# Kernel tuning notes

Hardware: AMD Instinct MI355X
Metric: run time of the kernel (lower is better)

Reference implementation:

```python
import jax, jax.numpy as jnp
import numpy as np

B, C, H, W = 8, 256, 64, 64
NH, KD, AG, PS, MIP = 8, 32, 64, 8, 8   # heads, key_dim, agent_num, pool_size, mip
EPS = 1e-5
SCALE = KD ** -0.5


def _bn(x, p):
    # p: [4, C] rows = (gamma, beta, mean, var); inference-mode BatchNorm2d, x: [B,C,H,W]
    g, b, m, v = p[0], p[1], p[2], p[3]
    inv = g * jax.lax.rsqrt(v + EPS)
    return x * inv[:, None, None] + (b - m * inv)[:, None, None]


def _conv1x1_bn(x, w, p):
    # 1x1 conv (no bias) + BN; act is Identity (the torch Conv act assignment is
    # overwritten by the else-branch, so even act='silu' ends up Identity)
    return _bn(jnp.einsum('bchw,oc->bohw', x, w), p)


def setup_inputs() -> dict:
    key = jax.random.key(0)
    ks = jax.random.split(key, 12)
    s = 0.05
    return {
        'x':       jax.random.normal(ks[0], (B, C, H, W), jnp.float32),
        'w_qkv':   jax.random.normal(ks[1], (3 * C, C), jnp.float32) * s,
        'bn_qkv':  jax.random.uniform(ks[2], (4, 3 * C), jnp.float32, 0.5, 1.5),
        'w_cv1':   jax.random.normal(ks[3], (MIP, C), jnp.float32) * s,
        'bn_cv1':  jax.random.uniform(ks[4], (4, MIP), jnp.float32, 0.5, 1.5),
        'w_cv2':   jax.random.normal(ks[5], (C, MIP), jnp.float32) * s,
        'bn_cv2':  jax.random.uniform(ks[6], (4, C), jnp.float32, 0.5, 1.5),
        'w_proj':  jax.random.normal(ks[7], (C, C), jnp.float32) * s,
        'bn_proj': jax.random.uniform(ks[8], (4, C), jnp.float32, 0.5, 1.5),
        'w_pe':    jax.random.normal(ks[9], (C, 1, 3, 3), jnp.float32) * s,
        'bn_pe':   jax.random.uniform(ks[10], (4, C), jnp.float32, 0.5, 1.5),
    }


def reference(x, w_qkv, bn_qkv, w_cv1, bn_cv1, w_cv2, bn_cv2,
              w_proj, bn_proj, w_pe, bn_pe):
    N = H * W
    qkv = _conv1x1_bn(x, w_qkv, bn_qkv)                     # [B,3C,H,W]
    q, k, v = jnp.split(qkv, 3, axis=1)                     # each [B,C,H,W]

    # direct == 'h': pool over W -> [B,C,H,1], SE-style gate via cv1->cv2, multiply
    a_k = k.mean(axis=3, keepdims=True)
    a_v = v.mean(axis=3, keepdims=True)
    k = _conv1x1_bn(_conv1x1_bn(a_k, w_cv1, bn_cv1), w_cv2, bn_cv2) * k
    v = _conv1x1_bn(_conv1x1_bn(a_v, w_cv1, bn_cv1), w_cv2, bn_cv2) * v

    # agent tokens: AdaptiveAvgPool2d to (PS,PS) == block-mean since H,W % PS == 0
    ap = q.reshape(B, C, PS, H // PS, PS, W // PS).mean(axis=(3, 5))  # [B,C,PS,PS]
    a = ap.reshape(B, NH, KD, AG)                            # [B,h,d,agent]

    qr = q.reshape(B, NH, KD, N)
    kr = k.reshape(B, NH, KD, N)
    vr = v.reshape(B, NH, KD, N)

    attn_k = jax.nn.softmax(jnp.einsum('bhda,bhdn->bhan', a, kr) * SCALE, axis=-1)  # [B,h,agent,N]
    attn = jnp.einsum('bhan,bhdn->bhad', attn_k, vr)                                # [B,h,agent,d]
    q_attn = jax.nn.softmax(jnp.einsum('bhdn,bhda->bhna', qr, a) * SCALE, axis=-1)  # [B,h,N,agent]
    out = jnp.einsum('bhna,bhad->bhdn', q_attn, attn).reshape(B, C, H, W)

    # depthwise 3x3 positional encoding on v, then BN
    pe = jax.lax.conv_general_dilated(
        v, w_pe, window_strides=(1, 1), padding='SAME',
        dimension_numbers=('NCHW', 'OIHW', 'NCHW'), feature_group_count=C)
    out = out + _bn(pe, bn_pe)

    return _conv1x1_bn(out, w_proj, bn_proj)
```

## Files before the change

### kernel.cpp

```cpp
#include <hip/hip_runtime.h>
#include <hip/hip_bf16.h>

#define NB 8
#define NC 256
#define NHW 4096
#define HDIM 64
#define WDIM 64
#define NHEAD 8
#define NKD 32
#define NAG 64
#define NMIP 8
#define NSPLIT 16
#define EPSF 1e-5f
#define FSCALE 0.17677669529663687f
#define SZQ ((size_t)NB * NC * NHW)

typedef __attribute__((ext_vector_type(8))) short bf16x8;
typedef __attribute__((ext_vector_type(8))) unsigned short u16x8;
typedef __attribute__((ext_vector_type(4))) unsigned short u16x4;
typedef __attribute__((ext_vector_type(4))) float f32x4;

__device__ __forceinline__ unsigned short f2bf(float f) {
    union { float f; unsigned u; } v; v.f = f;
    unsigned r = v.u + 0x7FFF + ((v.u >> 16) & 1);
    return (unsigned short)(r >> 16);
}
__device__ __forceinline__ float b2f(unsigned short u) {
    union { unsigned u32; float f; } v; v.u32 = ((unsigned)u) << 16; return v.f;
}
__device__ __forceinline__ void gload_lds16(const unsigned short* g, unsigned short* l) {
    __builtin_amdgcn_global_load_lds(
        (const __attribute__((address_space(1))) unsigned int*)g,
        (__attribute__((address_space(3))) unsigned int*)l, 16, 0, 0);
}

__global__ __launch_bounds__(256) void k_xpose(const float* __restrict__ x,
                                               unsigned short* __restrict__ xbt) {
    const int b = blockIdx.y;
    const int n0 = blockIdx.x * 64;
    const int tid = threadIdx.x;
    __shared__ unsigned short lt[64 * 258];

    #pragma unroll
    for (int it = 0; it < 4; ++it) {
        int c = it * 64 + (tid >> 2);
        int nq = (tid & 3) * 16;
        const float* xp = x + ((size_t)b * NC + c) * NHW + n0 + nq;
        float4 v0 = reinterpret_cast<const float4*>(xp)[0];
        float4 v1 = reinterpret_cast<const float4*>(xp)[1];
        float4 v2 = reinterpret_cast<const float4*>(xp)[2];
        float4 v3 = reinterpret_cast<const float4*>(xp)[3];
        float t[16] = {v0.x,v0.y,v0.z,v0.w, v1.x,v1.y,v1.z,v1.w,
                       v2.x,v2.y,v2.z,v2.w, v3.x,v3.y,v3.z,v3.w};
        #pragma unroll
        for (int i = 0; i < 16; ++i)
            lt[(nq + i) * 258 + c] = f2bf(t[i]);
    }
    __syncthreads();

    const int n = tid >> 2, cq = tid & 3;
    unsigned short* dst = xbt + ((size_t)b * NHW + n0 + n) * NC + cq * 64;
    #pragma unroll
    for (int v = 0; v < 8; ++v) {
        union { unsigned short u[8]; u16x8 w; } pk;
        #pragma unroll
        for (int i = 0; i < 8; ++i)
            pk.u[i] = lt[n * 258 + cq * 64 + v * 8 + i];
        *reinterpret_cast<u16x8*>(dst + v * 8) = pk.w;
    }
}

__global__ __launch_bounds__(256) void k_wcast(const float* __restrict__ wq,
                                               const float* __restrict__ wp,
                                               unsigned short* __restrict__ wqb,
                                               unsigned short* __restrict__ wpb) {
    const int i = (blockIdx.x * 256 + threadIdx.x) * 4;
    const int NQ = 768 * 256;
    if (i < NQ) {
        float4 v = *reinterpret_cast<const float4*>(wq + i);
        u16x4 u = {f2bf(v.x), f2bf(v.y), f2bf(v.z), f2bf(v.w)};
        *reinterpret_cast<u16x4*>(wqb + i) = u;
    } else {
        int j = i - NQ;
        float4 v = *reinterpret_cast<const float4*>(wp + j);
        u16x4 u = {f2bf(v.x), f2bf(v.y), f2bf(v.z), f2bf(v.w)};
        *reinterpret_cast<u16x4*>(wpb + j) = u;
    }
}

__global__ __launch_bounds__(256) void k_qkv(const unsigned short* __restrict__ xbt,
                                             const unsigned short* __restrict__ wb,
                                             const float* __restrict__ bnp,
                                             unsigned short* __restrict__ Qb,
                                             unsigned short* __restrict__ Kb,
                                             unsigned short* __restrict__ Vb,
                                             float* __restrict__ AMK,
                                             float* __restrict__ AMV) {
    const int b   = blockIdx.z;
    const int ocB = blockIdx.y * 128;
    const int nB  = blockIdx.x * 128;
    const int tid = threadIdx.x;
    const int wv  = tid >> 6, lane = tid & 63;
    const int wm = wv >> 1, wn = wv & 1;
    const int lm = lane & 15, lg = lane >> 4;

    __shared__ __align__(16) unsigned short S[2][8192];

    f32x4 acc[4][4];
    #pragma unroll
    for (int i = 0; i < 4; ++i)
        #pragma unroll
        for (int j = 0; j < 4; ++j)
            acc[i][j] = (f32x4){0.f, 0.f, 0.f, 0.f};

    const int srow = lane >> 2;
    const int kl = ((lane & 3) ^ ((lane >> 3) & 3)) * 8;
    const size_t agbase = (size_t)(ocB + wv * 32 + srow) * 256 + kl;
    const size_t bgbase = ((size_t)b * NHW + nB + wv * 32 + srow) * NC + kl;
    const int sw = (lm >> 1) & 3;

    auto STAGE = [&](int buf, int k0) {
        #pragma unroll
        for (int j = 0; j < 2; ++j) {
            gload_lds16(wb + agbase + (size_t)j * 16 * 256 + k0, &S[buf][wv * 1024 + j * 512]);
            gload_lds16(xbt + bgbase + (size_t)j * 16 * NC + k0, &S[buf][4096 + wv * 1024 + j * 512]);
        }
    };

    STAGE(0, 0);
    asm volatile("s_waitcnt vmcnt(0)" ::: "memory");
    __builtin_amdgcn_s_barrier();
    __builtin_amdgcn_sched_barrier(0);

    int cur = 0;
    for (int t = 0; t < 8; ++t) {
        if (t < 7) STAGE(cur ^ 1, (t + 1) * 32);

        const unsigned short* As = &S[cur][0];
        const unsigned short* Bs = &S[cur][4096];
        bf16x8 af[4], bfr[4];
        #pragma unroll
        for (int mi = 0; mi < 4; ++mi)
            af[mi] = *reinterpret_cast<const bf16x8*>(&As[(wm * 64 + mi * 16 + lm) * 32 + (lg ^ sw) * 8]);
        #pragma unroll
        for (int ni = 0; ni < 4; ++ni)
            bfr[ni] = *reinterpret_cast<const bf16x8*>(&Bs[(wn * 64 + ni * 16 + lm) * 32 + (lg ^ sw) * 8]);
        #pragma unroll
        for (int mi = 0; mi < 4; ++mi)
            #pragma unroll
            for (int ni = 0; ni < 4; ++ni)
                acc[mi][ni] = __builtin_amdgcn_mfma_f32_16x16x32_bf16(af[mi], bfr[ni], acc[mi][ni], 0, 0, 0);

        if (t < 7) {
            asm volatile("s_waitcnt vmcnt(0)" ::: "memory");
            __builtin_amdgcn_s_barrier();
            __builtin_amdgcn_sched_barrier(0);
            cur ^= 1;
        }
    }

    const int h_sp = (nB >> 6) + wn;
    unsigned short* wep = &S[0][0] + wv * 1152;
    #pragma unroll
    for (int mi = 0; mi < 4; ++mi) {
        const int ocrow = ocB + wm * 64 + mi * 16;
        #pragma unroll
        for (int r = 0; r < 4; ++r) {
            int lo = lg * 4 + r;
            int oc = ocrow + lo;
            float g = bnp[0 * 768 + oc], be = bnp[1 * 768 + oc];
            float m = bnp[2 * 768 + oc], vv = bnp[3 * 768 + oc];
            float inv = g * rsqrtf(vv + EPSF);
            float bias = be - m * inv;
            #pragma unroll
            for (int ni = 0; ni < 4; ++ni)
                wep[lo * 72 + ni * 16 + lm] = f2bf(acc[mi][ni][r] * inv + bias);
        }
        #pragma unroll
        for (int it = 0; it < 2; ++it) {
            int row = it * 8 + (lane >> 3);
            int seg = lane & 7;
            u16x8 v = *reinterpret_cast<const u16x8*>(&wep[row * 72 + seg * 8]);
            int oc = ocrow + row;
            unsigned short* base; int oc2;
            if (oc < 256)      { base = Qb; oc2 = oc; }
            else if (oc < 512) { base = Kb; oc2 = oc - 256; }
            else               { base = Vb; oc2 = oc - 512; }
            *reinterpret_cast<u16x8*>(base + ((size_t)b * NC + oc2) * NHW + nB + wn * 64 + seg * 8) = v;
            if (ocrow >= 256) {
                float s = 0.f;
                #pragma unroll
                for (int j = 0; j < 8; ++j) s += b2f(v[j]);
                s += __shfl_xor(s, 1);
                s += __shfl_xor(s, 2);
                s += __shfl_xor(s, 4);
                if (seg == 0) {
                    float* am = (oc < 512) ? AMK : AMV;
                    am[((size_t)b * HDIM + h_sp) * NC + oc2] = s * (1.0f / 64.0f);
                }
            }
        }
    }
}

__global__ __launch_bounds__(256) void k_gatecomp(const float* __restrict__ AMK,
                                                  const float* __restrict__ AMV,
                                                  const float* __restrict__ w1,
                                                  const float* __restrict__ bn1,
                                                  const float* __restrict__ w2,
                                                  const float* __restrict__ bn2,
                                                  float* __restrict__ GK,
                                                  float* __restrict__ GV) {
    const int b = blockIdx.x >> 6;
    const int h = blockIdx.x & 63;
    const int c = threadIdx.x;
    __shared__ float am[NC];
    __shared__ float m1[NMIP];
    for (int pass = 0; pass < 2; ++pass) {
        am[c] = (pass ? AMV : AMK)[((size_t)b * HDIM + h) * NC + c];
        __syncthreads();
        if (c < NMIP) {
            float t = 0.f;
            for (int cc = 0; cc < NC; ++cc) t += w1[c * NC + cc] * am[cc];
            float g = bn1[0 * NMIP + c], be = bn1[1 * NMIP + c];
            float mm = bn1[2 * NMIP + c], vv = bn1[3 * NMIP + c];
            float inv = g * rsqrtf(vv + EPSF);
            m1[c] = t * inv + (be - mm * inv);
        }
        __syncthreads();
        {
            float t = 0.f;
            #pragma unroll
            for (int j = 0; j < NMIP; ++j) t += w2[c * NMIP + j] * m1[j];
            float g = bn2[0 * NC + c], be = bn2[1 * NC + c];
            float mm = bn2[2 * NC + c], vv = bn2[3 * NC + c];
            float inv = g * rsqrtf(vv + EPSF);
            (pass ? GV : GK)[((size_t)b * NC + c) * HDIM + h] = t * inv + (be - mm * inv);
        }
        __syncthreads();
    }
}

__global__ __launch_bounds__(64) void k_pool(const unsigned short* __restrict__ Q,
                                             float* __restrict__ A_) {
    const int bc = blockIdx.x;
    const int ag = threadIdx.x;
    const int ph = ag >> 3, pw = ag & 7;
    const unsigned short* src = Q + (size_t)bc * NHW;
    float s = 0.f;
    #pragma unroll
    for (int i = 0; i < 8; ++i) {
        u16x8 v = *reinterpret_cast<const u16x8*>(&src[(ph * 8 + i) * WDIM + pw * 8]);
        #pragma unroll
        for (int j = 0; j < 8; ++j) s += b2f(v[j]);
    }
    A_[(size_t)bc * NAG + ag] = s * (1.0f / 64.0f);
}

__global__ __launch_bounds__(256) void k_attn_part(const unsigned short* __restrict__ K,
                                                   const unsigned short* __restrict__ V,
                                                   const float* __restrict__ A_,
                                                   const float* __restrict__ GK,
                                                   const float* __restrict__ GV,
                                                   float* __restrict__ Pm,
                                                   float* __restrict__ Pl,
                                                   float* __restrict__ Pacc) {
    const int bh = blockIdx.x >> 4;
    const int ns = blockIdx.x & (NSPLIT - 1);
    const int b = bh >> 3, h = bh & 7;
    const int tid = threadIdx.x;
    const int wv = tid >> 6, lane = tid & 63;
    const int lm = lane & 15, lg = lane >> 4;

    __shared__ unsigned short a_s[64 * 40];
    __shared__ unsigned short kt_s[64 * 40];
    __shared__ unsigned short vt_s[32 * 72];
    __shared__ unsigned short Ps[64 * 72];

    {
        int d = tid >> 3, ag0 = (tid & 7) * 8;
        const float* ap = A_ + ((size_t)(b * NC + h * NKD + d)) * NAG + ag0;
        float4 v0 = reinterpret_cast<const float4*>(ap)[0];
        float4 v1 = reinterpret_cast<const float4*>(ap)[1];
        float t8[8] = {v0.x, v0.y, v0.z, v0.w, v1.x, v1.y, v1.z, v1.w};
        #pragma unroll
        for (int i = 0; i < 8; ++i)
            a_s[(ag0 + i) * 40 + d] = f2bf(t8[i] * FSCALE);
    }

    float mrow[4], lrow[4];
    f32x4 acc[2];
    #pragma unroll
    for (int r = 0; r < 4; ++r) { mrow[r] = -1e30f; lrow[r] = 0.f; }
    acc[0] = (f32x4){0.f, 0.f, 0.f, 0.f};
    acc[1] = (f32x4){0.f, 0.f, 0.f, 0.f};

    const int colbase = ns * (NHW / NSPLIT);
    const unsigned short* Kp = K + (size_t)(b * NC + h * NKD) * NHW + colbase;
    const unsigned short* Vp = V + (size_t)(b * NC + h * NKD) * NHW + colbase;
    const int sd = tid >> 3;
    const size_t gbase = ((size_t)(b * NC + h * NKD + sd)) * HDIM;
    __syncthreads();

    for (int nt = 0; nt < 4; ++nt) {
        const int gh = ns * 4 + nt;
        {
            int c0 = tid & 7;
            float gk = GK[gbase + gh];
            const unsigned short* kp = Kp + (size_t)sd * NHW + nt * 64 + c0;
            #pragma unroll
            for (int i = 0; i < 8; ++i)
                kt_s[(c0 + 8 * i) * 40 + sd] = f2bf(b2f(kp[8 * i]) * gk);
        }
        {
            int c0 = (tid & 7) * 8;
            float gv = GV[gbase + gh];
            const unsigned short* vp = Vp + (size_t)sd * NHW + nt * 64 + c0;
            u16x8 vr = *reinterpret_cast<const u16x8*>(vp);
            union { unsigned short u[8]; u16x8 v; } pk;
            #pragma unroll
            for (int i = 0; i < 8; ++i) pk.u[i] = f2bf(b2f(vr[i]) * gv);
            *reinterpret_cast<u16x8*>(&vt_s[sd * 72 + c0]) = pk.v;
        }
        __syncthreads();

        f32x4 s[4];
        {
            bf16x8 af = *reinterpret_cast<const bf16x8*>(&a_s[(wv * 16 + lm) * 40 + lg * 8]);
            #pragma unroll
            for (int ni = 0; ni < 4; ++ni) {
                bf16x8 kf = *reinterpret_cast<const bf16x8*>(&kt_s[(ni * 16 + lm) * 40 + lg * 8]);
                s[ni] = __builtin_amdgcn_mfma_f32_16x16x32_bf16(
                    af, kf, (f32x4){0.f, 0.f, 0.f, 0.f}, 0, 0, 0);
            }
        }

        float fsc[4];
        #pragma unroll
        for (int r = 0; r < 4; ++r) {
            float mx = fmaxf(fmaxf(s[0][r], s[1][r]), fmaxf(s[2][r], s[3][r]));
            mx = fmaxf(mx, __shfl_xor(mx, 1));
            mx = fmaxf(mx, __shfl_xor(mx, 2));
            mx = fmaxf(mx, __shfl_xor(mx, 4));
            mx = fmaxf(mx, __shfl_xor(mx, 8));
            float mnew = fmaxf(mrow[r], mx);
            fsc[r] = __expf(mrow[r] - mnew);
            mrow[r] = mnew;
            int agrow = wv * 16 + lg * 4 + r;
            float ps = 0.f;
            #pragma unroll
            for (int ni = 0; ni < 4; ++ni) {
                float p = __expf(s[ni][r] - mnew);
                Ps[agrow * 72 + ni * 16 + lm] = f2bf(p);
                ps += p;
            }
            ps += __shfl_xor(ps, 1);
            ps += __shfl_xor(ps, 2);
            ps += __shfl_xor(ps, 4);
            ps += __shfl_xor(ps, 8);
            lrow[r] = lrow[r] * fsc[r] + ps;
        }
        #pragma unroll
        for (int ni = 0; ni < 2; ++ni)
            #pragma unroll
            for (int r = 0; r < 4; ++r)
                acc[ni][r] *= fsc[r];
        __syncthreads();

        #pragma unroll
        for (int kk = 0; kk < 2; ++kk) {
            bf16x8 pa = *reinterpret_cast<const bf16x8*>(&Ps[(wv * 16 + lm) * 72 + kk * 32 + lg * 8]);
            #pragma unroll
            for (int ni = 0; ni < 2; ++ni) {
                bf16x8 vb = *reinterpret_cast<const bf16x8*>(&vt_s[(ni * 16 + lm) * 72 + kk * 32 + lg * 8]);
                acc[ni] = __builtin_amdgcn_mfma_f32_16x16x32_bf16(pa, vb, acc[ni], 0, 0, 0);
            }
        }
        __syncthreads();
    }

    const size_t pbase = (size_t)(bh * NSPLIT + ns) * NAG;
    #pragma unroll
    for (int r = 0; r < 4; ++r) {
        int ag = wv * 16 + lg * 4 + r;
        #pragma unroll
        for (int ni = 0; ni < 2; ++ni)
            Pacc[(pbase + ag) * NKD + ni * 16 + lm] = acc[ni][r];
        if (lm == 0) {
            Pm[pbase + ag] = mrow[r];
            Pl[pbase + ag] = lrow[r];
        }
    }
}

__global__ __launch_bounds__(256) void k_attn_comb(const float* __restrict__ Pm,
                                                   const float* __restrict__ Pl,
                                                   const float* __restrict__ Pacc,
                                                   float* __restrict__ AT) {
    const int bh = blockIdx.x;
    const int tid = threadIdx.x;
    const int ag = tid >> 2, jg = tid & 3;
    float m = -1e30f;
    #pragma unroll
    for (int ns = 0; ns < NSPLIT; ++ns)
        m = fmaxf(m, Pm[(size_t)(bh * NSPLIT + ns) * NAG + ag]);
    float l = 0.f;
    float acc[8] = {};
    for (int ns = 0; ns < NSPLIT; ++ns) {
        size_t pb = (size_t)(bh * NSPLIT + ns) * NAG + ag;
        float f = __expf(Pm[pb] - m);
        l += Pl[pb] * f;
        const float* pp = Pacc + pb * NKD + jg * 8;
        #pragma unroll
        for (int i = 0; i < 8; ++i) acc[i] += pp[i] * f;
    }
    float linv = 1.0f / l;
    #pragma unroll
    for (int i = 0; i < 8; ++i)
        AT[((size_t)bh * NAG + ag) * NKD + jg * 8 + i] = acc[i] * linv;
}

__global__ __launch_bounds__(256) void k_qattn(const unsigned short* __restrict__ Q,
                                               const float* __restrict__ A_,
                                               const float* __restrict__ AT,
                                               unsigned short* __restrict__ O1t) {
    const int bh = blockIdx.y;
    const int b = bh >> 3, h = bh & 7;
    const int n0 = blockIdx.x * 128;
    const int tid = threadIdx.x;
    const int wv = tid >> 6, lane = tid & 63;
    const int lm = lane & 15, lg = lane >> 4;

    __shared__ unsigned short Qs[128][40];
    __shared__ unsigned short Ags[64][40];
    __shared__ unsigned short ATs[32][72];
    __shared__ unsigned short Ps[128][72];

    const unsigned short* Qbase = Q + ((size_t)b * NC + h * NKD) * NHW;

    {
        int d = tid >> 3, nb_ = (tid & 7) * 16;
        const unsigned short* qp = Qbase + (size_t)d * NHW + n0 + nb_;
        u16x8 v0 = *reinterpret_cast<const u16x8*>(qp);
        u16x8 v1 = *reinterpret_cast<const u16x8*>(qp + 8);
        #pragma unroll
        for (int i = 0; i < 8; ++i) Qs[nb_ + i][d] = v0[i];
        #pragma unroll
        for (int i = 0; i < 8; ++i) Qs[nb_ + 8 + i][d] = v1[i];
    }
    if (tid < 128) {
        int d = tid >> 2, ag0 = (tid & 3) * 16;
        const float* ap = A_ + ((size_t)(b * NC + h * NKD + d)) * NAG + ag0;
        #pragma unroll
        for (int i = 0; i < 16; ++i) Ags[ag0 + i][d] = f2bf(ap[i] * FSCALE);
    }
    if (tid < 128) {
        int ag = tid >> 1, d0 = (tid & 1) * 16;
        const float* atp = AT + ((size_t)bh * NAG + ag) * NKD + d0;
        #pragma unroll
        for (int i = 0; i < 16; ++i) ATs[d0 + i][ag] = f2bf(atp[i]);
    }
    __syncthreads();

    f32x4 s[2][4];
    #pragma unroll
    for (int mi = 0; mi < 2; ++mi)
        #pragma unroll
        for (int ni = 0; ni < 4; ++ni)
            s[mi][ni] = (f32x4){0.f, 0.f, 0.f, 0.f};
    {
        bf16x8 qa[2], ab[4];
        #pragma unroll
        for (int mi = 0; mi < 2; ++mi)
            qa[mi] = *reinterpret_cast<const bf16x8*>(&Qs[wv * 32 + mi * 16 + lm][lg * 8]);
        #pragma unroll
        for (int ni = 0; ni < 4; ++ni)
            ab[ni] = *reinterpret_cast<const bf16x8*>(&Ags[ni * 16 + lm][lg * 8]);
        #pragma unroll
        for (int mi = 0; mi < 2; ++mi)
            #pragma unroll
            for (int ni = 0; ni < 4; ++ni)
                s[mi][ni] = __builtin_amdgcn_mfma_f32_16x16x32_bf16(qa[mi], ab[ni], s[mi][ni], 0, 0, 0);
    }

    float lsum[2][4];
    #pragma unroll
    for (int mi = 0; mi < 2; ++mi) {
        #pragma unroll
        for (int r = 0; r < 4; ++r) {
            float mx = fmaxf(fmaxf(s[mi][0][r], s[mi][1][r]), fmaxf(s[mi][2][r], s[mi][3][r]));
            mx = fmaxf(mx, __shfl_xor(mx, 1));
            mx = fmaxf(mx, __shfl_xor(mx, 2));
            mx = fmaxf(mx, __shfl_xor(mx, 4));
            mx = fmaxf(mx, __shfl_xor(mx, 8));
            int nrow = wv * 32 + mi * 16 + lg * 4 + r;
            float ls = 0.f;
            #pragma unroll
            for (int ni = 0; ni < 4; ++ni) {
                float p = __expf(s[mi][ni][r] - mx);
                ls += p;
                Ps[nrow][ni * 16 + lm] = f2bf(p);
            }
            ls += __shfl_xor(ls, 1);
            ls += __shfl_xor(ls, 2);
            ls += __shfl_xor(ls, 4);
            ls += __shfl_xor(ls, 8);
            lsum[mi][r] = ls;
        }
    }
    __syncthreads();

    f32x4 o[2][2];
    #pragma unroll
    for (int mi = 0; mi < 2; ++mi)
        #pragma unroll
        for (int ni = 0; ni < 2; ++ni)
            o[mi][ni] = (f32x4){0.f, 0.f, 0.f, 0.f};
    #pragma unroll
    for (int kk = 0; kk < 2; ++kk) {
        bf16x8 pa[2], vb[2];
        #pragma unroll
        for (int mi = 0; mi < 2; ++mi)
            pa[mi] = *reinterpret_cast<const bf16x8*>(&Ps[wv * 32 + mi * 16 + lm][kk * 32 + lg * 8]);
        #pragma unroll
        for (int ni = 0; ni < 2; ++ni)
            vb[ni] = *reinterpret_cast<const bf16x8*>(&ATs[ni * 16 + lm][kk * 32 + lg * 8]);
        #pragma unroll
        for (int mi = 0; mi < 2; ++mi)
            #pragma unroll
            for (int ni = 0; ni < 2; ++ni)
                o[mi][ni] = __builtin_amdgcn_mfma_f32_16x16x32_bf16(pa[mi], vb[ni], o[mi][ni], 0, 0, 0);
    }

    unsigned short* obase = O1t + ((size_t)b * NHW + n0) * NC + h * NKD;
    #pragma unroll
    for (int mi = 0; mi < 2; ++mi) {
        #pragma unroll
        for (int r = 0; r < 4; ++r) {
            float rl = 1.0f / lsum[mi][r];
            int n = wv * 32 + mi * 16 + lg * 4 + r;
            #pragma unroll
            for (int ni = 0; ni < 2; ++ni) {
                int d = ni * 16 + lm;
                obase[(size_t)n * NC + d] = f2bf(o[mi][ni][r] * rl);
            }
        }
    }
}

__global__ __launch_bounds__(256) void k_pe(const unsigned short* __restrict__ V,
                                            const float* __restrict__ GV,
                                            const float* __restrict__ wpe,
                                            const float* __restrict__ bnp,
                                            unsigned short* __restrict__ O1t) {
    const int bh_ = blockIdx.x;
    const int b = bh_ >> 6, h = bh_ & 63;
    const int tid = threadIdx.x;
    __shared__ unsigned short vs[64 * 198];
    __shared__ float gvs[64][3];
    __shared__ float wps[64][9];
    __shared__ float bns[64][2];
    const int cl = tid & 63;
    const int wq = tid >> 6;

    for (int cc = 0; cc < 4; ++cc) {
        const int cbase = cc * 64;
        #pragma unroll
        for (int j = 0; j < 6; ++j) {
            int vecid = tid + 256 * j;
            int row = vecid >> 3, seg = vecid & 7;
            int c = row / 3, kh = row - c * 3;
            int hh = h + kh - 1;
            union { unsigned short u[8]; u16x8 w; } pk;
            if (hh >= 0 && hh < HDIM) {
                pk.w = *reinterpret_cast<const u16x8*>(
                    V + ((size_t)b * NC + cbase + c) * NHW + hh * WDIM + seg * 8);
            } else {
                #pragma unroll
                for (int i = 0; i < 8; ++i) pk.u[i] = 0;
            }
            *reinterpret_cast<u16x8*>(&vs[c * 198 + kh * 66 + 1 + seg * 8]) = pk.w;
        }
        if (tid < 192) {
            int c = tid / 3, kh = tid - c * 3;
            vs[c * 198 + kh * 66 + 0] = 0;
            vs[c * 198 + kh * 66 + 65] = 0;
            int hh = h + kh - 1;
            gvs[c][kh] = (hh >= 0 && hh < HDIM)
                ? GV[((size_t)b * NC + cbase + c) * HDIM + hh] : 0.f;
        }
        for (int i = tid; i < 64 * 9; i += 256)
            wps[i / 9][i % 9] = wpe[(cbase + i / 9) * 9 + i % 9];
        if (tid < 64) {
            int c = cbase + tid;
            float g = bnp[c], be = bnp[NC + c], m = bnp[2 * NC + c], vv = bnp[3 * NC + c];
            float inv = g * rsqrtf(vv + EPSF);
            bns[tid][0] = inv;
            bns[tid][1] = be - m * inv;
        }
        __syncthreads();

        float wr[9];
        #pragma unroll
        for (int i = 0; i < 9; ++i) wr[i] = wps[cl][i];
        float g0 = gvs[cl][0], g1 = gvs[cl][1], g2 = gvs[cl][2];
        float inv = bns[cl][0], bias = bns[cl][1];
        const unsigned short* vrow = &vs[cl * 198];
        unsigned short* obase = O1t + ((size_t)b * NHW + h * WDIM) * NC + cbase + cl;
        #pragma unroll
        for (int wi = 0; wi < 16; ++wi) {
            int w = wq * 16 + wi;
            float s0 = wr[0] * b2f(vrow[0 * 66 + w]) + wr[1] * b2f(vrow[0 * 66 + w + 1]) + wr[2] * b2f(vrow[0 * 66 + w + 2]);
            float s1 = wr[3] * b2f(vrow[1 * 66 + w]) + wr[4] * b2f(vrow[1 * 66 + w + 1]) + wr[5] * b2f(vrow[1 * 66 + w + 2]);
            float s2 = wr[6] * b2f(vrow[2 * 66 + w]) + wr[7] * b2f(vrow[2 * 66 + w + 1]) + wr[8] * b2f(vrow[2 * 66 + w + 2]);
            float s = s0 * g0 + s1 * g1 + s2 * g2;
            size_t oidx = (size_t)w * NC;
            obase[oidx] = f2bf(b2f(obase[oidx]) + s * inv + bias);
        }
        __syncthreads();
    }
}

__global__ __launch_bounds__(256) void k_proj(const unsigned short* __restrict__ O1t,
                                              const unsigned short* __restrict__ wb,
                                              const float* __restrict__ bnp,
                                              float* __restrict__ out) {
    const int b   = blockIdx.z;
    const int ocB = blockIdx.y * 128;
    const int nB  = blockIdx.x * 128;
    const int tid = threadIdx.x;
    const int wv  = tid >> 6, lane = tid & 63;
    const int wm = wv >> 1, wn = wv & 1;
    const int lm = lane & 15, lg = lane >> 4;

    __shared__ __align__(16) unsigned short S[2][8192];
    __shared__ float inv_s[128], bias_s[128];

    if (tid < 128) {
        int oc = ocB + tid;
        float g = bnp[0 * NC + oc], be = bnp[1 * NC + oc];
        float m = bnp[2 * NC + oc], vv = bnp[3 * NC + oc];
        float inv = g * rsqrtf(vv + EPSF);
        inv_s[tid] = inv;
        bias_s[tid] = be - m * inv;
    }

    f32x4 acc[4][4];
    #pragma unroll
    for (int i = 0; i < 4; ++i)
        #pragma unroll
        for (int j = 0; j < 4; ++j)
            acc[i][j] = (f32x4){0.f, 0.f, 0.f, 0.f};

    const int srow = lane >> 2;
    const int kl = ((lane & 3) ^ ((lane >> 3) & 3)) * 8;
    const size_t agbase = (size_t)(ocB + wv * 32 + srow) * 256 + kl;
    const size_t bgbase = ((size_t)b * NHW + nB + wv * 32 + srow) * NC + kl;
    const int sw = (lm >> 1) & 3;

    auto STAGE = [&](int buf, int k0) {
        #pragma unroll
        for (int j = 0; j < 2; ++j) {
            gload_lds16(wb + agbase + (size_t)j * 16 * 256 + k0, &S[buf][wv * 1024 + j * 512]);
            gload_lds16(O1t + bgbase + (size_t)j * 16 * NC + k0, &S[buf][4096 + wv * 1024 + j * 512]);
        }
    };

    STAGE(0, 0);
    asm volatile("s_waitcnt vmcnt(0)" ::: "memory");
    __builtin_amdgcn_s_barrier();
    __builtin_amdgcn_sched_barrier(0);

    int cur = 0;
    for (int t = 0; t < 8; ++t) {
        if (t < 7) STAGE(cur ^ 1, (t + 1) * 32);

        const unsigned short* As = &S[cur][0];
        const unsigned short* Bs = &S[cur][4096];
        bf16x8 af[4], bfr[4];
        #pragma unroll
        for (int mi = 0; mi < 4; ++mi)
            af[mi] = *reinterpret_cast<const bf16x8*>(&As[(wm * 64 + mi * 16 + lm) * 32 + (lg ^ sw) * 8]);
        #pragma unroll
        for (int ni = 0; ni < 4; ++ni)
            bfr[ni] = *reinterpret_cast<const bf16x8*>(&Bs[(wn * 64 + ni * 16 + lm) * 32 + (lg ^ sw) * 8]);
        #pragma unroll
        for (int mi = 0; mi < 4; ++mi)
            #pragma unroll
            for (int ni = 0; ni < 4; ++ni)
                acc[mi][ni] = __builtin_amdgcn_mfma_f32_16x16x32_bf16(af[mi], bfr[ni], acc[mi][ni], 0, 0, 0);

        if (t < 7) {
            asm volatile("s_waitcnt vmcnt(0)" ::: "memory");
            __builtin_amdgcn_s_barrier();
            __builtin_amdgcn_sched_barrier(0);
            cur ^= 1;
        }
    }

    float* dstb = out + ((size_t)b * NC + ocB) * NHW + nB;
    #pragma unroll
    for (int mi = 0; mi < 4; ++mi) {
        int lo_base = wm * 64 + mi * 16 + lg * 4;
        #pragma unroll
        for (int r = 0; r < 4; ++r) {
            int lo = lo_base + r;
            float inv = inv_s[lo], bias = bias_s[lo];
            #pragma unroll
            for (int ni = 0; ni < 4; ++ni) {
                int n = wn * 64 + ni * 16 + lm;
                dstb[(size_t)lo * NHW + n] = acc[mi][ni][r] * inv + bias;
            }
        }
    }
}

extern "C" void kernel_launch(void* const* d_in, const int* in_sizes, int n_in,
                              void* d_out, int out_size, void* d_ws, size_t ws_size,
                              hipStream_t stream) {
    (void)in_sizes; (void)n_in; (void)out_size; (void)ws_size;
    const float* x       = (const float*)d_in[0];
    const float* w_qkv   = (const float*)d_in[1];
    const float* bn_qkv  = (const float*)d_in[2];
    const float* w_cv1   = (const float*)d_in[3];
    const float* bn_cv1  = (const float*)d_in[4];
    const float* w_cv2   = (const float*)d_in[5];
    const float* bn_cv2  = (const float*)d_in[6];
    const float* w_proj  = (const float*)d_in[7];
    const float* bn_proj = (const float*)d_in[8];
    const float* w_pe    = (const float*)d_in[9];
    const float* bn_pe   = (const float*)d_in[10];
    float* out = (float*)d_out;

    unsigned short* Qb  = (unsigned short*)d_ws;
    unsigned short* Kb  = Qb + SZQ;
    unsigned short* Vb  = Kb + SZQ;
    unsigned short* O1t = Vb + SZQ;
    unsigned short* xbt = O1t + SZQ;
    unsigned short* wqb = xbt + SZQ;
    unsigned short* wpb = wqb + 768 * 256;
    float* Aa   = (float*)(wpb + 65536);
    float* AT   = Aa + (size_t)NB * NC * NAG;
    float* Pm   = AT + (size_t)NB * NHEAD * NAG * NKD;
    float* Pl   = Pm + (size_t)NB * NHEAD * NSPLIT * NAG;
    float* Pacc = Pl + (size_t)NB * NHEAD * NSPLIT * NAG;
    float* AMK  = Pacc + (size_t)NB * NHEAD * NSPLIT * NAG * NKD;
    float* AMV  = AMK + (size_t)NB * HDIM * NC;
    float* GK   = AMV + (size_t)NB * HDIM * NC;
    float* GV   = GK + (size_t)NB * NC * HDIM;

    k_xpose<<<dim3(64, NB), 256, 0, stream>>>(x, xbt);
    k_wcast<<<256, 256, 0, stream>>>(w_qkv, w_proj, wqb, wpb);
    k_qkv<<<dim3(32, 6, NB), 256, 0, stream>>>(xbt, wqb, bn_qkv, Qb, Kb, Vb, AMK, AMV);
    k_gatecomp<<<NB * HDIM, 256, 0, stream>>>(AMK, AMV, w_cv1, bn_cv1, w_cv2, bn_cv2, GK, GV);
    k_pool<<<NB * NC, 64, 0, stream>>>(Qb, Aa);
    k_attn_part<<<NB * NHEAD * NSPLIT, 256, 0, stream>>>(Kb, Vb, Aa, GK, GV, Pm, Pl, Pacc);
    k_attn_comb<<<NB * NHEAD, 256, 0, stream>>>(Pm, Pl, Pacc, AT);
    k_qattn<<<dim3(32, 64), 256, 0, stream>>>(Qb, Aa, AT, O1t);
    k_pe<<<NB * HDIM, 256, 0, stream>>>(Vb, GV, w_pe, bn_pe, O1t);
    k_proj<<<dim3(32, 2, NB), 256, 0, stream>>>(O1t, wpb, bn_proj, out);
}
```

Measured before the change: 142.8 us.

## Triple-buffer QKV GEMM loads and defer V gate to after PV MFMA

```diff
diff --git a/kernel.cpp b/kernel.cpp
--- a/kernel.cpp
+++ b/kernel.cpp
@@ -104,7 +104,7 @@
     const int wm = wv >> 1, wn = wv & 1;
     const int lm = lane & 15, lg = lane >> 4;
 
-    __shared__ __align__(16) unsigned short S[2][8192];
+    __shared__ __align__(16) unsigned short S[3][8192];
 
     f32x4 acc[4][4];
     #pragma unroll
@@ -128,16 +128,20 @@
     };
 
     STAGE(0, 0);
-    asm volatile("s_waitcnt vmcnt(0)" ::: "memory");
-    __builtin_amdgcn_s_barrier();
-    __builtin_amdgcn_sched_barrier(0);
-
-    int cur = 0;
+    STAGE(1, 32);
+
+    #pragma unroll
     for (int t = 0; t < 8; ++t) {
-        if (t < 7) STAGE(cur ^ 1, (t + 1) * 32);
-
-        const unsigned short* As = &S[cur][0];
-        const unsigned short* Bs = &S[cur][4096];
+        if (t <= 5) STAGE((t + 2) % 3, (t + 2) * 32);
+
+        if (t <= 5)      asm volatile("s_waitcnt vmcnt(8)" ::: "memory");
+        else if (t == 6) asm volatile("s_waitcnt vmcnt(4)" ::: "memory");
+        else             asm volatile("s_waitcnt vmcnt(0)" ::: "memory");
+        __builtin_amdgcn_s_barrier();
+        __builtin_amdgcn_sched_barrier(0);
+
+        const unsigned short* As = &S[t % 3][0];
+        const unsigned short* Bs = &S[t % 3][4096];
         bf16x8 af[4], bfr[4];
         #pragma unroll
         for (int mi = 0; mi < 4; ++mi)
@@ -151,11 +155,9 @@
             for (int ni = 0; ni < 4; ++ni)
                 acc[mi][ni] = __builtin_amdgcn_mfma_f32_16x16x32_bf16(af[mi], bfr[ni], acc[mi][ni], 0, 0, 0);
 
-        if (t < 7) {
-            asm volatile("s_waitcnt vmcnt(0)" ::: "memory");
+        if (t <= 4) {
             __builtin_amdgcn_s_barrier();
             __builtin_amdgcn_sched_barrier(0);
-            cur ^= 1;
         }
     }
 
@@ -314,13 +316,9 @@
         }
         {
             int c0 = (tid & 7) * 8;
-            float gv = GV[gbase + gh];
             const unsigned short* vp = Vp + (size_t)sd * NHW + nt * 64 + c0;
-            u16x8 vr = *reinterpret_cast<const u16x8*>(vp);
-            union { unsigned short u[8]; u16x8 v; } pk;
-            #pragma unroll
-            for (int i = 0; i < 8; ++i) pk.u[i] = f2bf(b2f(vr[i]) * gv);
-            *reinterpret_cast<u16x8*>(&vt_s[sd * 72 + c0]) = pk.v;
+            *reinterpret_cast<u16x8*>(&vt_s[sd * 72 + c0]) =
+                *reinterpret_cast<const u16x8*>(vp);
         }
         __syncthreads();
 
@@ -367,14 +365,24 @@
                 acc[ni][r] *= fsc[r];
         __syncthreads();
 
+        f32x4 pv[2];
+        pv[0] = (f32x4){0.f, 0.f, 0.f, 0.f};
+        pv[1] = (f32x4){0.f, 0.f, 0.f, 0.f};
         #pragma unroll
         for (int kk = 0; kk < 2; ++kk) {
             bf16x8 pa = *reinterpret_cast<const bf16x8*>(&Ps[(wv * 16 + lm) * 72 + kk * 32 + lg * 8]);
             #pragma unroll
             for (int ni = 0; ni < 2; ++ni) {
                 bf16x8 vb = *reinterpret_cast<const bf16x8*>(&vt_s[(ni * 16 + lm) * 72 + kk * 32 + lg * 8]);
-                acc[ni] = __builtin_amdgcn_mfma_f32_16x16x32_bf16(pa, vb, acc[ni], 0, 0, 0);
+                pv[ni] = __builtin_amdgcn_mfma_f32_16x16x32_bf16(pa, vb, pv[ni], 0, 0, 0);
             }
+        }
+        #pragma unroll
+        for (int ni = 0; ni < 2; ++ni) {
+            float gv = GV[((size_t)(b * NC + h * NKD + ni * 16 + lm)) * HDIM + gh];
+            #pragma unroll
+            for (int r = 0; r < 4; ++r)
+                acc[ni][r] = fmaf(gv, pv[ni][r], acc[ni][r]);
         }
         __syncthreads();
     }
```

Measured after the change: 143.8 us. Within noise of the previous version (+0.7%).
